# Kernel tuning notes

Measured on AMD Instinct MI355X. Metric: run time of the kernel, lower is better.

The kernel has to match this reference:

```python
import jax, jax.numpy as jnp
from jax import lax
import numpy as np

B = 16384
EPS = 1e-5


def conv2d(x, w, b, pad):
    # x: [N,C,H,W], w: [O,I,kh,kw]
    y = lax.conv_general_dilated(x, w, (1, 1), [(pad, pad), (pad, pad)],
                                 dimension_numbers=("NCHW", "OIHW", "NCHW"))
    return y + b[None, :, None, None]


def maxpool2(x):
    return lax.reduce_window(x, -jnp.inf, lax.max, (1, 1, 2, 2), (1, 1, 2, 2), "VALID")


def setup_inputs() -> dict:
    key = jax.random.key(0)
    ks = jax.random.split(key, 16)
    n = jax.random.normal
    return {
        "x": n(ks[0], (B, 1, 28, 28), dtype=jnp.float32),
        "conv1_w": n(ks[1], (8, 1, 3, 3), dtype=jnp.float32) * 0.2,
        "conv1_b": n(ks[2], (8,), dtype=jnp.float32) * 0.1,
        "conv2_w": n(ks[3], (16, 8, 3, 3), dtype=jnp.float32) * 0.1,
        "conv2_b": n(ks[4], (16,), dtype=jnp.float32) * 0.1,
        "s1_w": n(ks[5], (4, 2), dtype=jnp.float32) * 0.5,
        "s1_b": n(ks[6], (4,), dtype=jnp.float32) * 0.1,
        "s2_w": n(ks[7], (2, 4), dtype=jnp.float32) * 0.5,
        "s2_b": n(ks[8], (2,), dtype=jnp.float32) * 0.1,
        "filt_w": n(ks[9], (1, 1, 2, 2), dtype=jnp.float32) * 0.5,
        "filt_b": n(ks[10], (1,), dtype=jnp.float32) * 0.1,
        "fc1_w": n(ks[11], (64, 787), dtype=jnp.float32) * 0.03,
        "fc1_b": n(ks[12], (64,), dtype=jnp.float32) * 0.1,
        "fc2_w": n(ks[13], (4, 64), dtype=jnp.float32) * 0.1,
        "fc2_b": n(ks[14], (4,), dtype=jnp.float32) * 0.1,
        "bn_g": jnp.ones((4,), dtype=jnp.float32),
        "bn_b": jnp.zeros((4,), dtype=jnp.float32),
    }


def reference(x, conv1_w, conv1_b, conv2_w, conv2_b, s1_w, s1_b, s2_w, s2_b,
              filt_w, filt_b, fc1_w, fc1_b, fc2_w, fc2_b, bn_g, bn_b):
    bsz = x.shape[0]
    # feature extractor: conv3x3 -> relu -> maxpool2 (x2)
    f = maxpool2(jax.nn.relu(conv2d(x, conv1_w, conv1_b, 1)))        # [B,8,14,14]
    f = maxpool2(jax.nn.relu(conv2d(f, conv2_w, conv2_b, 1)))        # [B,16,7,7]
    flat = f.reshape(bsz, -1)                                        # [B,784]
    # sampler on first two features
    h = jnp.tanh(flat[:, :2] @ s1_w.T + s1_b)
    sampler_out = jax.nn.softmax(h @ s2_w.T + s2_b, axis=-1)         # [B,2]
    # conv filter: 2x2 stride-1 conv + sigmoid, mean over all patches
    logits = conv2d(x, filt_w, filt_b, 0)                            # [B,1,27,27]
    conv_out = jnp.mean(jax.nn.sigmoid(logits), axis=(1, 2, 3))[:, None]  # [B,1]
    combined = jnp.concatenate([flat, sampler_out, conv_out], axis=1)  # [B,787]
    out = jax.nn.relu(combined @ fc1_w.T + fc1_b) @ fc2_w.T + fc2_b    # [B,4]
    # BatchNorm1d, training mode (batch stats, biased variance)
    mu = jnp.mean(out, axis=0)
    var = jnp.var(out, axis=0)
    return (out - mu) * lax.rsqrt(var + EPS) * bn_g + bn_b
```

## Files before the change

### kernel.cpp

```cpp
#include <hip/hip_runtime.h>
#include <hip/hip_fp16.h>
#include <math.h>

#define NBATCH 16384
#define EPSV 1e-5f

typedef short short8 __attribute__((ext_vector_type(8)));
typedef _Float16 half8_t __attribute__((ext_vector_type(8)));
typedef short short2v __attribute__((ext_vector_type(2)));
typedef float f32x4 __attribute__((ext_vector_type(4)));
union V8 { uint4 u; short8 s; };
union VH { uint4 u; half8_t h; };

__device__ __forceinline__ unsigned short f2bf(float f) {
    unsigned int x = __float_as_uint(f);
    return (unsigned short)((x + 0x7fffu + ((x >> 16) & 1u)) >> 16);
}
__device__ __forceinline__ __half2 u2h(unsigned int u) { return __builtin_bit_cast(__half2, u); }
__device__ __forceinline__ unsigned int h2u(__half2 h) { return __builtin_bit_cast(unsigned int, h); }

__global__ __launch_bounds__(256) void k_prep(
    const float* __restrict__ fc1w, const float* __restrict__ w2,
    const float* __restrict__ w1, const float* __restrict__ b1,
    unsigned short* __restrict__ wt, unsigned short* __restrict__ af16,
    unsigned int* __restrict__ w1h2, unsigned int* __restrict__ b1h2)
{
    int i = blockIdx.x * 256 + threadIdx.x;
    if (i < 51200) {
        int n = i / 800, k = i - n * 800;
        float v = (k < 787) ? fc1w[n * 787 + k] : 0.f;
        wt[i] = f2bf(v);
    } else if (i < 52736) {
        int a = i - 51200;
        int slot = a >> 7, rem = a & 127, oc = rem >> 3, ic = rem & 7;
        float v = (slot < 9) ? w2[oc * 72 + ic * 9 + slot] : 0.f;
        af16[a] = __half_as_ushort(__float2half(v));
    } else if (i < 52808) {
        int k = i - 52736;
        unsigned int hb = __half_as_ushort(__float2half(w1[k]));
        w1h2[k] = hb | (hb << 16);
    } else if (i < 52816) {
        int k = i - 52808;
        unsigned int hb = __half_as_ushort(__float2half(b1[k]));
        b1h2[k] = hb | (hb << 16);
    }
}

#define SXS 15
#define WPB 2

__global__ __launch_bounds__(128, 6) void k_conv(
    const float* __restrict__ x,
    const float* __restrict__ s1w, const float* __restrict__ s1b,
    const float* __restrict__ s2w, const float* __restrict__ s2b,
    const float* __restrict__ fw, const float* __restrict__ fb,
    const float* __restrict__ b2,
    const unsigned short* __restrict__ Afg,
    const unsigned int* __restrict__ w1h2g,
    const unsigned int* __restrict__ b1h2g,
    unsigned short* __restrict__ comb)
{
    const int t = threadIdx.x;
    const int w = t >> 6, l = t & 63;

    __shared__ unsigned int sxu_all[WPB][30 * SXS];
    __shared__ __align__(16) unsigned short sf1_all[WPB][16 * 136];
    __shared__ float ssm[27];
    __shared__ float sb2s[16];

    unsigned int* sxu = sxu_all[w];
    unsigned short* sf1 = sf1_all[w];

    if (t < 8) ssm[t] = s1w[t];
    else if (t < 12) ssm[t] = s1b[t - 8];
    else if (t < 20) ssm[t] = s2w[t - 12];
    else if (t < 22) ssm[t] = s2b[t - 20];
    else if (t < 26) ssm[t] = fw[t - 22];
    else if (t == 26) ssm[26] = fb[0];
    if (t >= 32 && t < 48) sb2s[t - 32] = b2[t - 32];
    __syncthreads();

    for (int i = l; i < 30 * SXS; i += 64) sxu[i] = 0u;
    if (l < 60) {
        int R, C;
        if (l < 16)      { R = 0;      C = l; }
        else if (l < 32) { R = 15;     C = l - 16; }
        else if (l < 46) { R = l - 31; C = 0; }
        else             { R = l - 45; C = 15; }
        *reinterpret_cast<uint4*>(&sf1[R * 136 + C * 8]) = uint4{0u, 0u, 0u, 0u};
    }

    const __half2 fwh0 = __float2half2_rn(ssm[22]);
    const __half2 fwh1 = __float2half2_rn(ssm[23]);
    const __half2 fwh2 = __float2half2_rn(ssm[24]);
    const __half2 fwh3 = __float2half2_rn(ssm[25]);
    const __half2 fbh  = __float2half2_rn(ssm[26]);

    const int n = l & 15, g = l >> 4;
    const int qr = n & 7;
    const int q = (qr < 7) ? qr : 6;
    const int dr = n >> 3;
    int offs[3];
    VH af[3];
    #pragma unroll
    for (int s = 0; s < 3; ++s) {
        const int slot = s * 4 + g;
        const int u = slot / 3, v = slot - 3 * (slot / 3);
        offs[s] = (slot <= 8) ? (u * 136 + v * 8) : 0;
        af[s].u = *reinterpret_cast<const uint4*>(Afg + ((slot * 16 + n) << 3));
    }
    float biasv[4];
    #pragma unroll
    for (int i = 0; i < 4; ++i) biasv[i] = sb2s[4 * g + i];

    int srow[7], sww[7];
    #pragma unroll
    for (int k = 0; k < 7; ++k) {
        int u0 = l + k * 64;
        srow[k] = u0 / 15;
        sww[k]  = u0 - srow[k] * 15;
    }

    const int b = blockIdx.x * WPB + w;
    const float* xb = x + (size_t)b * 784;
    unsigned short* crow = comb + (size_t)b * 800;

    float xlo[7], xhi[7];
    #pragma unroll
    for (int k = 0; k < 7; ++k) {
        const int u0 = l + k * 64;
        if (u0 < 420) {
            const float* base = xb + srow[k] * 28;
            xlo[k] = (sww[k] == 0)  ? 0.f : base[2 * sww[k] - 1];
            xhi[k] = (sww[k] == 14) ? 0.f : base[2 * sww[k]];
        }
    }
    #pragma unroll
    for (int k = 0; k < 7; ++k) {
        const int u0 = l + k * 64;
        if (u0 < 420)
            sxu[(srow[k] + 1) * SXS + sww[k]] = h2u(__floats2half2_rn(xlo[k], xhi[k]));
    }

    float fsum = 0.f;
    for (int u0 = l; u0 < 378; u0 += 64) {
        int r = u0 / 14, cp = u0 - (u0 / 14) * 14;
        unsigned int A1 = sxu[(r + 1) * SXS + cp], B1 = sxu[(r + 1) * SXS + cp + 1];
        unsigned int A2 = sxu[(r + 2) * SXS + cp], B2 = sxu[(r + 2) * SXS + cp + 1];
        __half2 al1 = u2h(__builtin_amdgcn_alignbit(B1, A1, 16));
        __half2 al2 = u2h(__builtin_amdgcn_alignbit(B2, A2, 16));
        __half2 acc = __hfma2(fwh0, al1,
                      __hfma2(fwh1, u2h(B1),
                      __hfma2(fwh2, al2,
                      __hfma2(fwh3, u2h(B2), fbh))));
        float2 f = __half22float2(acc);
        fsum += __frcp_rn(1.f + __expf(-f.x));
        if (cp < 13) fsum += __frcp_rn(1.f + __expf(-f.y));
    }
    #pragma unroll
    for (int off = 32; off > 0; off >>= 1)
        fsum += __shfl_xor(fsum, off, 64);

    for (int i = l; i < 196; i += 64) {
        const int p = i / 14, j = i - (i / 14) * 14;
        unsigned int A[4], B[4], M[4];
        #pragma unroll
        for (int u = 0; u < 4; ++u) {
            A[u] = sxu[(2 * p + u) * SXS + j];
            B[u] = sxu[(2 * p + u) * SXS + j + 1];
            M[u] = __builtin_amdgcn_alignbit(B[u], A[u], 16);
        }
        unsigned short outv[8];
        #pragma unroll
        for (int oc = 0; oc < 8; ++oc) {
            __half2 a0 = u2h(b1h2g[oc]), a1 = a0;
            #pragma unroll
            for (int u = 0; u < 3; ++u) {
                #pragma unroll
                for (int v = 0; v < 3; ++v) {
                    const __half2 wv = u2h(w1h2g[oc * 9 + u * 3 + v]);
                    const unsigned int p0 = (v == 0) ? A[u]     : ((v == 1) ? M[u]     : B[u]);
                    const unsigned int p1 = (v == 0) ? A[u + 1] : ((v == 1) ? M[u + 1] : B[u + 1]);
                    a0 = __hfma2(wv, u2h(p0), a0);
                    a1 = __hfma2(wv, u2h(p1), a1);
                }
            }
            short2v s0 = __builtin_bit_cast(short2v, a0);
            short2v s1 = __builtin_bit_cast(short2v, a1);
            short2v mm = __builtin_elementwise_max(s0, s1);
            short m = mm[0] > mm[1] ? mm[0] : mm[1];
            if (m < 0) m = 0;
            outv[oc] = (unsigned short)m;
        }
        *reinterpret_cast<uint4*>(&sf1[(p + 1) * 136 + (j + 1) * 8]) =
            *reinterpret_cast<const uint4*>(outv);
    }

    float f0r = 0.f, f1r = 0.f;
    for (int pp = 0; pp < 7; ++pp) {
        const int rbase = (2 * pp + dr) * 136 + (2 * q) * 8;
        f32x4 acc0 = {0.f, 0.f, 0.f, 0.f}, acc1 = {0.f, 0.f, 0.f, 0.f};
        #pragma unroll
        for (int s = 0; s < 3; ++s) {
            VH b0, b1v;
            b0.u  = *reinterpret_cast<const uint4*>(&sf1[rbase + offs[s]]);
            b1v.u = *reinterpret_cast<const uint4*>(&sf1[rbase + 8 + offs[s]]);
            acc0 = __builtin_amdgcn_mfma_f32_16x16x32_f16(af[s].h, b0.h, acc0, 0, 0, 0);
            acc1 = __builtin_amdgcn_mfma_f32_16x16x32_f16(af[s].h, b1v.h, acc1, 0, 0, 0);
        }
        #pragma unroll
        for (int i = 0; i < 4; ++i) {
            float m = fmaxf(acc0[i], acc1[i]);
            m = fmaxf(m, __shfl_xor(m, 8, 64));
            float val = fmaxf(m + biasv[i], 0.f);
            if (pp == 0 && i == 0) {
                f0r = __shfl(val, 0, 64);
                f1r = __shfl(val, 1, 64);
            }
            if (n < 7)
                crow[(4 * g + i) * 49 + pp * 7 + q] = f2bf(val);
        }
    }

    if (l < 13) crow[787 + l] = 0;
    if (l == 0) {
        crow[786] = f2bf(fsum * (1.f / 729.f));
        float h[4];
        #pragma unroll
        for (int k = 0; k < 4; ++k) {
            float y = fmaf(f0r, ssm[k * 2], fmaf(f1r, ssm[k * 2 + 1], ssm[8 + k]));
            float e = __expf(2.f * y);
            h[k] = (e - 1.f) * __frcp_rn(e + 1.f);
        }
        float l0 = ssm[20], l1 = ssm[21];
        #pragma unroll
        for (int k = 0; k < 4; ++k) {
            l0 = fmaf(h[k], ssm[12 + k], l0);
            l1 = fmaf(h[k], ssm[16 + k], l1);
        }
        float mx = fmaxf(l0, l1);
        float e0 = __expf(l0 - mx), e1 = __expf(l1 - mx);
        float inv = __frcp_rn(e0 + e1);
        crow[784] = f2bf(e0 * inv);
        crow[785] = f2bf(e1 * inv);
    }
}

__global__ __launch_bounds__(256) void k_fc(
    const unsigned short* __restrict__ A,
    const unsigned short* __restrict__ Bw,
    const float* __restrict__ fc1b,
    const float* __restrict__ fc2w, const float* __restrict__ fc2b,
    float* __restrict__ out, float* __restrict__ part)
{
    __shared__ uint4 Asm[2][256];
    __shared__ uint4 Bsm[2][256];
    __shared__ float sh[64][68];
    __shared__ float sfc2[4][64];
    __shared__ float pacc[4][8];

    const int t = threadIdx.x;
    const int w = t >> 6, l = t & 63;
    const int blk = blockIdx.x;

    sfc2[t >> 6][t & 63] = fc2w[t];

    const int srow = t >> 2, skbp = t & 3;
    const int skbl = skbp ^ ((srow >> 1) & 3);
    const uint4* Ag = reinterpret_cast<const uint4*>(A) + ((size_t)blk * 64 + srow) * 100;
    const uint4* Bg = reinterpret_cast<const uint4*>(Bw) + (size_t)srow * 100;
    const int sidx = srow * 4 + skbp;

    const int arow = w * 16 + (l & 15);
    const int aidx = arow * 4 + ((l >> 4) ^ ((arow >> 1) & 3));
    int bidx[4];
    #pragma unroll
    for (int nf = 0; nf < 4; ++nf) {
        int nn = nf * 16 + (l & 15);
        bidx[nf] = nn * 4 + ((l >> 4) ^ ((nn >> 1) & 3));
    }

    f32x4 acc0 = {0.f, 0.f, 0.f, 0.f}, acc1 = acc0, acc2 = acc0, acc3 = acc0;

    Asm[0][sidx] = Ag[skbl];
    Bsm[0][sidx] = Bg[skbl];

    int buf = 0;
    for (int s = 0; s < 25; ++s) {
        __syncthreads();
        if (s < 24) {
            Asm[buf ^ 1][sidx] = Ag[(s + 1) * 4 + skbl];
            Bsm[buf ^ 1][sidx] = Bg[(s + 1) * 4 + skbl];
        }
        V8 av; av.u = Asm[buf][aidx];
        V8 b0; b0.u = Bsm[buf][bidx[0]];
        V8 b1; b1.u = Bsm[buf][bidx[1]];
        V8 b2; b2.u = Bsm[buf][bidx[2]];
        V8 b3; b3.u = Bsm[buf][bidx[3]];
        acc0 = __builtin_amdgcn_mfma_f32_16x16x32_bf16(av.s, b0.s, acc0, 0, 0, 0);
        acc1 = __builtin_amdgcn_mfma_f32_16x16x32_bf16(av.s, b1.s, acc1, 0, 0, 0);
        acc2 = __builtin_amdgcn_mfma_f32_16x16x32_bf16(av.s, b2.s, acc2, 0, 0, 0);
        acc3 = __builtin_amdgcn_mfma_f32_16x16x32_bf16(av.s, b3.s, acc3, 0, 0, 0);
        buf ^= 1;
    }

    {
        const int c0 = l & 15, r0 = w * 16 + (l >> 4) * 4;
        float fb0 = fc1b[c0], fb1 = fc1b[16 + c0], fb2 = fc1b[32 + c0], fb3 = fc1b[48 + c0];
        #pragma unroll
        for (int r = 0; r < 4; ++r) {
            sh[r0 + r][c0]      = fmaxf(acc0[r] + fb0, 0.f);
            sh[r0 + r][16 + c0] = fmaxf(acc1[r] + fb1, 0.f);
            sh[r0 + r][32 + c0] = fmaxf(acc2[r] + fb2, 0.f);
            sh[r0 + r][48 + c0] = fmaxf(acc3[r] + fb3, 0.f);
        }
    }
    __syncthreads();

    {
        const int row = t >> 2, oo = t & 3;
        float s = fc2b[oo];
        #pragma unroll 8
        for (int o = 0; o < 64; ++o)
            s = fmaf(sh[row][o], sfc2[oo][o], s);
        out[((size_t)blk * 64 + row) * 4 + oo] = s;

        float rs = s, rq = s * s;
        #pragma unroll
        for (int off = 4; off < 64; off <<= 1) {
            rs += __shfl_xor(rs, off, 64);
            rq += __shfl_xor(rq, off, 64);
        }
        if (l < 4) pacc[w][l] = rs;
        else if (l < 8) pacc[w][l] = rq;
    }
    __syncthreads();
    if (t < 8)
        part[blk * 8 + t] = pacc[0][t] + pacc[1][t] + pacc[2][t] + pacc[3][t];
}

__global__ void k_bnfinal(const float* __restrict__ part,
                          const float* __restrict__ g, const float* __restrict__ bb,
                          float* __restrict__ ss, int nblocks)
{
    const int t = threadIdx.x;
    float s[8];
    #pragma unroll
    for (int i = 0; i < 8; ++i) s[i] = 0.f;
    for (int idx = t; idx < nblocks; idx += 64)
        #pragma unroll
        for (int i = 0; i < 8; ++i) s[i] += part[idx * 8 + i];
    #pragma unroll
    for (int i = 0; i < 8; ++i)
        #pragma unroll
        for (int off = 32; off > 0; off >>= 1)
            s[i] += __shfl_xor(s[i], off, 64);
    if (t == 0) {
        const float invB = 1.f / 16384.f;
        #pragma unroll
        for (int j = 0; j < 4; ++j) {
            float mu = s[j] * invB;
            float var = s[4 + j] * invB - mu * mu;
            float sc = g[j] * rsqrtf(var + EPSV);
            ss[j] = sc;
            ss[4 + j] = bb[j] - mu * sc;
        }
    }
}

__global__ __launch_bounds__(256) void k_bnapply(const float* __restrict__ ss,
                                                 float* __restrict__ out)
{
    const int row = blockIdx.x * 256 + threadIdx.x;
    float4 v = reinterpret_cast<float4*>(out)[row];
    v.x = fmaf(v.x, ss[0], ss[4]);
    v.y = fmaf(v.y, ss[1], ss[5]);
    v.z = fmaf(v.z, ss[2], ss[6]);
    v.w = fmaf(v.w, ss[3], ss[7]);
    reinterpret_cast<float4*>(out)[row] = v;
}

__global__ __launch_bounds__(256) void k_transpose_fb(const float* __restrict__ in,
                                                      float* __restrict__ out)
{
    int i = blockIdx.x * 256 + threadIdx.x;
    if (i < 787 * 64) {
        int k = i >> 6, o = i & 63;
        out[i] = in[o * 787 + k];
    }
}

#define SF1F(ic, r, c) sf1[(ic) * 324 + (r) * 20 + (c)]

__global__ __launch_bounds__(256) void k_fused_fb(
    const float* __restrict__ x,
    const float* __restrict__ w1, const float* __restrict__ b1,
    const float* __restrict__ w2, const float* __restrict__ b2,
    const float* __restrict__ s1w, const float* __restrict__ s1b,
    const float* __restrict__ s2w, const float* __restrict__ s2b,
    const float* __restrict__ fw, const float* __restrict__ fb,
    const float* __restrict__ wt, const float* __restrict__ fc1b,
    const float* __restrict__ fc2w, const float* __restrict__ fc2b,
    float* __restrict__ pre)
{
    const int b = blockIdx.x;
    const int t = threadIdx.x;

    __shared__ float sxA[30][20];
    __shared__ float sxB[30][20];
    __shared__ float sf1[8 * 324];
    __shared__ float scomb[788];
    __shared__ float sw1[72];
    __shared__ float sb1[8];
    __shared__ float sw2p[16 * 76];
    __shared__ float sb2[16];
    __shared__ float sh1p[4][64];
    __shared__ float sh1[64];
    __shared__ float sred[4];
    __shared__ float ssm[27];

    for (int i = t; i < 600; i += 256) { (&sxA[0][0])[i] = 0.f; (&sxB[0][0])[i] = 0.f; }
    for (int i = t; i < 8 * 324; i += 256) sf1[i] = 0.f;
    if (t < 72) sw1[t] = w1[t];
    if (t < 8) sb1[t] = b1[t];
    for (int i = t; i < 1152; i += 256) {
        int oc = i / 72, rem = i - oc * 72;
        sw2p[oc * 76 + rem] = w2[i];
    }
    if (t < 16) sb2[t] = b2[t];
    if (t < 8) ssm[t] = s1w[t];
    else if (t < 12) ssm[t] = s1b[t - 8];
    else if (t < 20) ssm[t] = s2w[t - 12];
    else if (t < 22) ssm[t] = s2b[t - 20];
    else if (t < 26) ssm[t] = fw[t - 22];
    else if (t == 26) ssm[t] = fb[0];
    __syncthreads();

    const float* xb = x + (size_t)b * 784;
    for (int i = t; i < 784; i += 256) {
        int r = i / 28, c = i - (i / 28) * 28;
        float v = xb[i];
        int pr = r + 1, pc = c + 1;
        if (pc <= 15) sxA[pr][pc] = v;
        if (pc >= 14) sxB[pr][pc - 14] = v;
    }
    __syncthreads();

    {
        const float fw00 = ssm[22], fw01 = ssm[23], fw10 = ssm[24], fw11 = ssm[25];
        const float fbv = ssm[26];
        float fsum = 0.f;
        for (int i = t; i < 729; i += 256) {
            int r = i / 27, c = i - (i / 27) * 27;
            float x00, x01, x10, x11;
            if (c <= 13) {
                x00 = sxA[r + 1][c + 1]; x01 = sxA[r + 1][c + 2];
                x10 = sxA[r + 2][c + 1]; x11 = sxA[r + 2][c + 2];
            } else {
                int cb = c - 14;
                x00 = sxB[r + 1][cb + 1]; x01 = sxB[r + 1][cb + 2];
                x10 = sxB[r + 2][cb + 1]; x11 = sxB[r + 2][cb + 2];
            }
            float v = fbv;
            v = fmaf(x00, fw00, v); v = fmaf(x01, fw01, v);
            v = fmaf(x10, fw10, v); v = fmaf(x11, fw11, v);
            fsum += 1.f / (1.f + expf(-v));
        }
        #pragma unroll
        for (int off = 32; off > 0; off >>= 1)
            fsum += __shfl_xor(fsum, off, 64);
        if ((t & 63) == 0) sred[t >> 6] = fsum;
    }

    {
        const int half = t >> 7;
        const int id = t & 127;
        if (id < 112) {
            const int p = id >> 3, oc = id & 7;
            const float* base = half ? &sxB[0][0] : &sxA[0][0];
            float X[4][16];
            #pragma unroll
            for (int u = 0; u < 4; ++u) {
                const float4* rp = reinterpret_cast<const float4*>(base + (2 * p + u) * 20);
                float4 a = rp[0], bb4 = rp[1], c4 = rp[2], d4 = rp[3];
                X[u][0] = a.x;  X[u][1] = a.y;  X[u][2] = a.z;  X[u][3] = a.w;
                X[u][4] = bb4.x; X[u][5] = bb4.y; X[u][6] = bb4.z; X[u][7] = bb4.w;
                X[u][8] = c4.x;  X[u][9] = c4.y;  X[u][10] = c4.z; X[u][11] = c4.w;
                X[u][12] = d4.x; X[u][13] = d4.y; X[u][14] = d4.z; X[u][15] = d4.w;
            }
            float W[9];
            #pragma unroll
            for (int k = 0; k < 9; ++k) W[k] = sw1[oc * 9 + k];
            const float bias = sb1[oc];
            const int j0 = half * 7;
            #pragma unroll
            for (int jj = 0; jj < 7; ++jj) {
                float m = 0.f;
                #pragma unroll
                for (int dr = 0; dr < 2; ++dr)
                    #pragma unroll
                    for (int dc = 0; dc < 2; ++dc) {
                        float acc = bias;
                        #pragma unroll
                        for (int u = 0; u < 3; ++u)
                            #pragma unroll
                            for (int v = 0; v < 3; ++v)
                                acc = fmaf(X[dr + u][2 * jj + dc + v], W[u * 3 + v], acc);
                        m = fmaxf(m, acc);
                    }
                SF1F(oc, p + 1, j0 + jj + 1) = m;
            }
        }
    }
    __syncthreads();

    if (t < 112) {
        const int p = t >> 4, oc = t & 15;
        const float bias = sb2[oc];
        float acc[7][4];
        #pragma unroll
        for (int jj = 0; jj < 7; ++jj)
            #pragma unroll
            for (int s = 0; s < 4; ++s) acc[jj][s] = bias;
        for (int ic = 0; ic < 8; ++ic) {
            float X[4][16];
            #pragma unroll
            for (int u = 0; u < 4; ++u) {
                const float4* rp = reinterpret_cast<const float4*>(&SF1F(ic, 2 * p + u, 0));
                float4 a = rp[0], bb4 = rp[1], c4 = rp[2], d4 = rp[3];
                X[u][0] = a.x;  X[u][1] = a.y;  X[u][2] = a.z;  X[u][3] = a.w;
                X[u][4] = bb4.x; X[u][5] = bb4.y; X[u][6] = bb4.z; X[u][7] = bb4.w;
                X[u][8] = c4.x;  X[u][9] = c4.y;  X[u][10] = c4.z; X[u][11] = c4.w;
                X[u][12] = d4.x; X[u][13] = d4.y; X[u][14] = d4.z; X[u][15] = d4.w;
            }
            float W[9];
            #pragma unroll
            for (int k = 0; k < 9; ++k) W[k] = sw2p[oc * 76 + ic * 9 + k];
            #pragma unroll
            for (int jj = 0; jj < 7; ++jj)
                #pragma unroll
                for (int dr = 0; dr < 2; ++dr)
                    #pragma unroll
                    for (int dc = 0; dc < 2; ++dc)
                        #pragma unroll
                        for (int u = 0; u < 3; ++u)
                            #pragma unroll
                            for (int v = 0; v < 3; ++v)
                                acc[jj][dr * 2 + dc] =
                                    fmaf(X[dr + u][2 * jj + dc + v], W[u * 3 + v], acc[jj][dr * 2 + dc]);
        }
        #pragma unroll
        for (int jj = 0; jj < 7; ++jj) {
            float m = fmaxf(fmaxf(acc[jj][0], acc[jj][1]), fmaxf(acc[jj][2], acc[jj][3]));
            scomb[oc * 49 + p * 7 + jj] = fmaxf(m, 0.f);
        }
    }
    __syncthreads();

    if (t == 0) {
        scomb[786] = (sred[0] + sred[1] + sred[2] + sred[3]) * (1.f / 729.f);
        float f0 = scomb[0], f1 = scomb[1];
        float h[4];
        #pragma unroll
        for (int k = 0; k < 4; ++k)
            h[k] = tanhf(fmaf(f0, ssm[k * 2], fmaf(f1, ssm[k * 2 + 1], ssm[8 + k])));
        float l0 = ssm[20], l1 = ssm[21];
        #pragma unroll
        for (int k = 0; k < 4; ++k) {
            l0 = fmaf(h[k], ssm[12 + k], l0);
            l1 = fmaf(h[k], ssm[16 + k], l1);
        }
        float mx = fmaxf(l0, l1);
        float e0 = expf(l0 - mx), e1 = expf(l1 - mx);
        float inv = 1.f / (e0 + e1);
        scomb[784] = e0 * inv;
        scomb[785] = e1 * inv;
    }
    __syncthreads();

    {
        const int o = t & 63, w = t >> 6;
        const int k0 = w * 197;
        const int k1 = (w == 3) ? 787 : k0 + 197;
        const float* wp = wt + (size_t)k0 * 64 + o;
        float acc = 0.f;
        #pragma unroll 4
        for (int k = k0; k < k1; ++k) {
            acc = fmaf(scomb[k], *wp, acc);
            wp += 64;
        }
        sh1p[w][o] = acc;
    }
    __syncthreads();
    if (t < 64)
        sh1[t] = fmaxf(sh1p[0][t] + sh1p[1][t] + sh1p[2][t] + sh1p[3][t] + fc1b[t], 0.f);
    __syncthreads();

    {
        const int oo = t >> 6, lane = t & 63;
        float v = sh1[lane] * fc2w[oo * 64 + lane];
        #pragma unroll
        for (int off = 32; off > 0; off >>= 1)
            v += __shfl_xor(v, off, 64);
        if (lane == 0) pre[(size_t)b * 4 + oo] = v + fc2b[oo];
    }
}

__global__ __launch_bounds__(256) void k_bnstat_fb(const float* __restrict__ pre,
                                                   float* __restrict__ part)
{
    const int t = threadIdx.x;
    const int row = blockIdx.x * 256 + t;
    float4 v = reinterpret_cast<const float4*>(pre)[row];
    float s0 = v.x, s1 = v.y, s2 = v.z, s3 = v.w;
    float q0 = v.x * v.x, q1 = v.y * v.y, q2 = v.z * v.z, q3 = v.w * v.w;
    #pragma unroll
    for (int off = 32; off > 0; off >>= 1) {
        s0 += __shfl_xor(s0, off, 64);
        s1 += __shfl_xor(s1, off, 64);
        s2 += __shfl_xor(s2, off, 64);
        s3 += __shfl_xor(s3, off, 64);
        q0 += __shfl_xor(q0, off, 64);
        q1 += __shfl_xor(q1, off, 64);
        q2 += __shfl_xor(q2, off, 64);
        q3 += __shfl_xor(q3, off, 64);
    }
    __shared__ float acc[4][8];
    if ((t & 63) == 0) {
        int w = t >> 6;
        acc[w][0] = s0; acc[w][1] = s1; acc[w][2] = s2; acc[w][3] = s3;
        acc[w][4] = q0; acc[w][5] = q1; acc[w][6] = q2; acc[w][7] = q3;
    }
    __syncthreads();
    if (t < 8)
        part[blockIdx.x * 8 + t] = acc[0][t] + acc[1][t] + acc[2][t] + acc[3][t];
}

extern "C" void kernel_launch(void* const* d_in, const int* in_sizes, int n_in,
                              void* d_out, int out_size, void* d_ws, size_t ws_size,
                              hipStream_t stream)
{
    const float* x    = (const float*)d_in[0];
    const float* w1   = (const float*)d_in[1];
    const float* b1   = (const float*)d_in[2];
    const float* w2   = (const float*)d_in[3];
    const float* b2   = (const float*)d_in[4];
    const float* s1w  = (const float*)d_in[5];
    const float* s1b  = (const float*)d_in[6];
    const float* s2w  = (const float*)d_in[7];
    const float* s2b  = (const float*)d_in[8];
    const float* fw   = (const float*)d_in[9];
    const float* fb   = (const float*)d_in[10];
    const float* fc1w = (const float*)d_in[11];
    const float* fc1b = (const float*)d_in[12];
    const float* fc2w = (const float*)d_in[13];
    const float* fc2b = (const float*)d_in[14];
    const float* bng  = (const float*)d_in[15];
    const float* bnb  = (const float*)d_in[16];

    float* out = (float*)d_out;

    const size_t COMB_BYTES = (size_t)NBATCH * 800 * 2;
    const size_t WT_BYTES   = 64 * 800 * 2;
    const size_t AF16_BYTES = 1536 * 2;
    const size_t W1H2_BYTES = 72 * 4;
    const size_t B1H2_BYTES = 8 * 4;
    const size_t PART_BYTES = 256 * 8 * 4;
    const size_t NEED = COMB_BYTES + WT_BYTES + AF16_BYTES + W1H2_BYTES +
                        B1H2_BYTES + PART_BYTES + 32;

    if (ws_size >= NEED) {
        char* p = (char*)d_ws;
        unsigned short* comb = (unsigned short*)p;                     p += COMB_BYTES;
        unsigned short* wtbf = (unsigned short*)p;                     p += WT_BYTES;
        unsigned short* af16 = (unsigned short*)p;                     p += AF16_BYTES;
        unsigned int*   w1h2 = (unsigned int*)p;                       p += W1H2_BYTES;
        unsigned int*   b1h2 = (unsigned int*)p;                       p += B1H2_BYTES;
        float*          part = (float*)p;                              p += PART_BYTES;
        float*          ss   = (float*)p;

        k_prep<<<207, 256, 0, stream>>>(fc1w, w2, w1, b1, wtbf, af16, w1h2, b1h2);
        k_conv<<<NBATCH / WPB, 128, 0, stream>>>(x, s1w, s1b, s2w, s2b, fw, fb, b2,
                                                 af16, w1h2, b1h2, comb);
        k_fc<<<256, 256, 0, stream>>>(comb, wtbf, fc1b, fc2w, fc2b, out, part);
        k_bnfinal<<<1, 64, 0, stream>>>(part, bng, bnb, ss, 256);
        k_bnapply<<<64, 256, 0, stream>>>(ss, out);
    } else {
        float* part = (float*)d_ws;
        float* ss   = part + 512;
        float* wt   = ss + 8;

        k_transpose_fb<<<197, 256, 0, stream>>>(fc1w, wt);
        k_fused_fb<<<NBATCH, 256, 0, stream>>>(x, w1, b1, w2, b2, s1w, s1b, s2w, s2b,
                                               fw, fb, wt, fc1b, fc2w, fc2b, out);
        k_bnstat_fb<<<64, 256, 0, stream>>>(out, part);
        k_bnfinal<<<1, 64, 0, stream>>>(part, bng, bnb, ss, 64);
        k_bnapply<<<64, 256, 0, stream>>>(ss, out);
    }
}
```

Measured before the change: 94.89 us.

## Use one-wave conv blocks, drop shared scalar staging, switch FC to fp16

The conv kernel now runs one 64-thread block per sample instead of two waves per block. This removes the shared-memory staging of small parameters and its __syncthreads, reading them directly from global memory instead, with a higher min-blocks launch bound. The combined activations and fc1 weights are stored as fp16 rather than bf16, and the FC GEMM uses the f16 MFMA variant. Extra precision is traded for a narrower range, which could overflow if activations are large. There are also twice as many tiny blocks to schedule.

```diff
diff --git a/kernel.cpp b/kernel.cpp
--- a/kernel.cpp
+++ b/kernel.cpp
@@ -16,6 +16,9 @@
     unsigned int x = __float_as_uint(f);
     return (unsigned short)((x + 0x7fffu + ((x >> 16) & 1u)) >> 16);
 }
+__device__ __forceinline__ unsigned short f2h(float f) {
+    return __half_as_ushort(__float2half(f));
+}
 __device__ __forceinline__ __half2 u2h(unsigned int u) { return __builtin_bit_cast(__half2, u); }
 __device__ __forceinline__ unsigned int h2u(__half2 h) { return __builtin_bit_cast(unsigned int, h); }
 
@@ -29,27 +32,26 @@
     if (i < 51200) {
         int n = i / 800, k = i - n * 800;
         float v = (k < 787) ? fc1w[n * 787 + k] : 0.f;
-        wt[i] = f2bf(v);
+        wt[i] = f2h(v);
     } else if (i < 52736) {
         int a = i - 51200;
         int slot = a >> 7, rem = a & 127, oc = rem >> 3, ic = rem & 7;
         float v = (slot < 9) ? w2[oc * 72 + ic * 9 + slot] : 0.f;
-        af16[a] = __half_as_ushort(__float2half(v));
+        af16[a] = f2h(v);
     } else if (i < 52808) {
         int k = i - 52736;
-        unsigned int hb = __half_as_ushort(__float2half(w1[k]));
+        unsigned int hb = f2h(w1[k]);
         w1h2[k] = hb | (hb << 16);
     } else if (i < 52816) {
         int k = i - 52808;
-        unsigned int hb = __half_as_ushort(__float2half(b1[k]));
+        unsigned int hb = f2h(b1[k]);
         b1h2[k] = hb | (hb << 16);
     }
 }
 
 #define SXS 15
-#define WPB 2
-
-__global__ __launch_bounds__(128, 6) void k_conv(
+
+__global__ __launch_bounds__(64, 8) void k_conv(
     const float* __restrict__ x,
     const float* __restrict__ s1w, const float* __restrict__ s1b,
     const float* __restrict__ s2w, const float* __restrict__ s2b,
@@ -60,25 +62,10 @@
     const unsigned int* __restrict__ b1h2g,
     unsigned short* __restrict__ comb)
 {
-    const int t = threadIdx.x;
-    const int w = t >> 6, l = t & 63;
-
-    __shared__ unsigned int sxu_all[WPB][30 * SXS];
-    __shared__ __align__(16) unsigned short sf1_all[WPB][16 * 136];
-    __shared__ float ssm[27];
-    __shared__ float sb2s[16];
-
-    unsigned int* sxu = sxu_all[w];
-    unsigned short* sf1 = sf1_all[w];
-
-    if (t < 8) ssm[t] = s1w[t];
-    else if (t < 12) ssm[t] = s1b[t - 8];
-    else if (t < 20) ssm[t] = s2w[t - 12];
-    else if (t < 22) ssm[t] = s2b[t - 20];
-    else if (t < 26) ssm[t] = fw[t - 22];
-    else if (t == 26) ssm[26] = fb[0];
-    if (t >= 32 && t < 48) sb2s[t - 32] = b2[t - 32];
-    __syncthreads();
+    const int l = threadIdx.x;
+
+    __shared__ unsigned int sxu[30 * SXS];
+    __shared__ __align__(16) unsigned short sf1[16 * 136];
 
     for (int i = l; i < 30 * SXS; i += 64) sxu[i] = 0u;
     if (l < 60) {
@@ -90,11 +77,11 @@
         *reinterpret_cast<uint4*>(&sf1[R * 136 + C * 8]) = uint4{0u, 0u, 0u, 0u};
     }
 
-    const __half2 fwh0 = __float2half2_rn(ssm[22]);
-    const __half2 fwh1 = __float2half2_rn(ssm[23]);
-    const __half2 fwh2 = __float2half2_rn(ssm[24]);
-    const __half2 fwh3 = __float2half2_rn(ssm[25]);
-    const __half2 fbh  = __float2half2_rn(ssm[26]);
+    const __half2 fwh0 = __float2half2_rn(fw[0]);
+    const __half2 fwh1 = __float2half2_rn(fw[1]);
+    const __half2 fwh2 = __float2half2_rn(fw[2]);
+    const __half2 fwh3 = __float2half2_rn(fw[3]);
+    const __half2 fbh  = __float2half2_rn(fb[0]);
 
     const int n = l & 15, g = l >> 4;
     const int qr = n & 7;
@@ -111,7 +98,7 @@
     }
     float biasv[4];
     #pragma unroll
-    for (int i = 0; i < 4; ++i) biasv[i] = sb2s[4 * g + i];
+    for (int i = 0; i < 4; ++i) biasv[i] = b2[4 * g + i];
 
     int srow[7], sww[7];
     #pragma unroll
@@ -121,7 +108,7 @@
         sww[k]  = u0 - srow[k] * 15;
     }
 
-    const int b = blockIdx.x * WPB + w;
+    const int b = blockIdx.x;
     const float* xb = x + (size_t)b * 784;
     unsigned short* crow = comb + (size_t)b * 800;
 
@@ -218,31 +205,31 @@
                 f1r = __shfl(val, 1, 64);
             }
             if (n < 7)
-                crow[(4 * g + i) * 49 + pp * 7 + q] = f2bf(val);
+                crow[(4 * g + i) * 49 + pp * 7 + q] = f2h(val);
         }
     }
 
     if (l < 13) crow[787 + l] = 0;
     if (l == 0) {
-        crow[786] = f2bf(fsum * (1.f / 729.f));
+        crow[786] = f2h(fsum * (1.f / 729.f));
         float h[4];
         #pragma unroll
         for (int k = 0; k < 4; ++k) {
-            float y = fmaf(f0r, ssm[k * 2], fmaf(f1r, ssm[k * 2 + 1], ssm[8 + k]));
+            float y = fmaf(f0r, s1w[2 * k], fmaf(f1r, s1w[2 * k + 1], s1b[k]));
             float e = __expf(2.f * y);
             h[k] = (e - 1.f) * __frcp_rn(e + 1.f);
         }
-        float l0 = ssm[20], l1 = ssm[21];
+        float l0 = s2b[0], l1 = s2b[1];
         #pragma unroll
         for (int k = 0; k < 4; ++k) {
-            l0 = fmaf(h[k], ssm[12 + k], l0);
-            l1 = fmaf(h[k], ssm[16 + k], l1);
+            l0 = fmaf(h[k], s2w[k], l0);
+            l1 = fmaf(h[k], s2w[4 + k], l1);
         }
         float mx = fmaxf(l0, l1);
         float e0 = __expf(l0 - mx), e1 = __expf(l1 - mx);
         float inv = __frcp_rn(e0 + e1);
-        crow[784] = f2bf(e0 * inv);
-        crow[785] = f2bf(e1 * inv);
+        crow[784] = f2h(e0 * inv);
+        crow[785] = f2h(e1 * inv);
     }
 }
 
@@ -292,15 +279,15 @@
             Asm[buf ^ 1][sidx] = Ag[(s + 1) * 4 + skbl];
             Bsm[buf ^ 1][sidx] = Bg[(s + 1) * 4 + skbl];
         }
-        V8 av; av.u = Asm[buf][aidx];
-        V8 b0; b0.u = Bsm[buf][bidx[0]];
-        V8 b1; b1.u = Bsm[buf][bidx[1]];
-        V8 b2; b2.u = Bsm[buf][bidx[2]];
-        V8 b3; b3.u = Bsm[buf][bidx[3]];
-        acc0 = __builtin_amdgcn_mfma_f32_16x16x32_bf16(av.s, b0.s, acc0, 0, 0, 0);
-        acc1 = __builtin_amdgcn_mfma_f32_16x16x32_bf16(av.s, b1.s, acc1, 0, 0, 0);
-        acc2 = __builtin_amdgcn_mfma_f32_16x16x32_bf16(av.s, b2.s, acc2, 0, 0, 0);
-        acc3 = __builtin_amdgcn_mfma_f32_16x16x32_bf16(av.s, b3.s, acc3, 0, 0, 0);
+        VH av; av.u = Asm[buf][aidx];
+        VH b0; b0.u = Bsm[buf][bidx[0]];
+        VH b1; b1.u = Bsm[buf][bidx[1]];
+        VH b2; b2.u = Bsm[buf][bidx[2]];
+        VH b3; b3.u = Bsm[buf][bidx[3]];
+        acc0 = __builtin_amdgcn_mfma_f32_16x16x32_f16(av.h, b0.h, acc0, 0, 0, 0);
+        acc1 = __builtin_amdgcn_mfma_f32_16x16x32_f16(av.h, b1.h, acc1, 0, 0, 0);
+        acc2 = __builtin_amdgcn_mfma_f32_16x16x32_f16(av.h, b2.h, acc2, 0, 0, 0);
+        acc3 = __builtin_amdgcn_mfma_f32_16x16x32_f16(av.h, b3.h, acc3, 0, 0, 0);
         buf ^= 1;
     }
 
@@ -680,8 +667,8 @@
         float*          ss   = (float*)p;
 
         k_prep<<<207, 256, 0, stream>>>(fc1w, w2, w1, b1, wtbf, af16, w1h2, b1h2);
-        k_conv<<<NBATCH / WPB, 128, 0, stream>>>(x, s1w, s1b, s2w, s2b, fw, fb, b2,
-                                                 af16, w1h2, b1h2, comb);
+        k_conv<<<NBATCH, 64, 0, stream>>>(x, s1w, s1b, s2w, s2b, fw, fb, b2,
+                                          af16, w1h2, b1h2, comb);
         k_fc<<<256, 256, 0, stream>>>(comb, wtbf, fc1b, fc2w, fc2b, out, part);
         k_bnfinal<<<1, 64, 0, stream>>>(part, bng, bnb, ss, 256);
         k_bnapply<<<64, 256, 0, stream>>>(ss, out);
```

New measurement: 90.32 us. 4.8% less time.
